# Performance work log

Hardware: AMD Instinct MI355X
Metric: run time of the kernel (lower is better)

Reference implementation:

```python
import jax, jax.numpy as jnp
import numpy as np

BN_EPS = 1e-5
LEAKY_SLOPE = 0.2


def setup_inputs() -> dict:
    key = jax.random.key(0)
    B, T, J, H = 32, 128, 24, 256
    ks = jax.random.split(key, 16)

    def w(k, shape, scale=0.05):
        return jax.random.normal(k, shape, dtype=jnp.float32) * scale

    return {
        "xt_seq": jax.random.normal(ks[0], (B, T, J * 3), dtype=jnp.float32),
        "tau_seq": jax.random.uniform(ks[1], (B, T, 1), dtype=jnp.float32),
        "z_seq": jax.random.normal(ks[2], (B, T, H), dtype=jnp.float32),
        "h_n": jax.random.normal(ks[3], (1, B, H), dtype=jnp.float32),
        "adj": jax.random.uniform(ks[4], (J, J), dtype=jnp.float32),
        # linear weights stored as [in, out] (transposed vs torch)
        "w_joint": w(ks[5], (3, H)), "b_joint": jnp.zeros((H,), jnp.float32),
        "w_t1": w(ks[6], (1, H)), "b_t1": jnp.zeros((H,), jnp.float32),
        "w_t2": w(ks[7], (H, H)), "b_t2": jnp.zeros((H,), jnp.float32),
        "w_radar": w(ks[8], (H, H)), "b_radar": jnp.zeros((H,), jnp.float32),
        "w_gcn": w(ks[9], (H, H)), "b_gcn": jnp.zeros((H,), jnp.float32),
        "w_conv": w(ks[10], (H, H, 3)), "b_conv": jnp.zeros((H,), jnp.float32),  # [out,in,k]
        "bn_gamma": jnp.ones((H,), jnp.float32), "bn_beta": jnp.zeros((H,), jnp.float32),
        "bn_mean": jnp.zeros((H,), jnp.float32), "bn_var": jnp.ones((H,), jnp.float32),
        "w_out": w(ks[11], (H, 3)), "b_out": jnp.zeros((3,), jnp.float32),
    }


def _forward(xt_seq, tau_seq, z_seq, h_n, adj,
             w_joint, b_joint, w_t1, b_t1, w_t2, b_t2,
             w_radar, b_radar, w_gcn, b_gcn, w_conv, b_conv,
             bn_gamma, bn_beta, bn_mean, bn_var, w_out, b_out):
    B, T, _ = xt_seq.shape
    J = adj.shape[0]
    H = w_radar.shape[0]

    x = xt_seq.reshape(B, T, J, 3)
    h = x @ w_joint + b_joint                                  # [B,T,J,H]

    t_emb = jax.nn.silu(tau_seq @ w_t1 + b_t1) @ w_t2 + b_t2   # [B,T,H]
    h = h + t_emb[:, :, None, :]

    z_proj = z_seq @ w_radar + b_radar                         # [B,T,H]
    h = h + z_proj[:, :, None, :]

    h_radar = h_n[0] @ w_radar + b_radar                       # [B,H]
    h = h + h_radar[:, None, None, :]

    # GCN adjacency aggregation + linear + relu residual
    h_gcn = jnp.einsum('jk,btkh->btjh', adj, h)
    h = h + jax.nn.relu(h_gcn @ w_gcn + b_gcn)

    # temporal conv over T: [B*J, H, T]
    h_t = h.transpose(0, 2, 3, 1).reshape(B * J, H, T)
    h_t = jax.lax.conv_general_dilated(
        h_t, w_conv, window_strides=(1,), padding=[(1, 1)],
        dimension_numbers=('NCH', 'OIH', 'NCH')) + b_conv[None, :, None]
    # BatchNorm1d in eval mode (running stats)
    scale = bn_gamma * jax.lax.rsqrt(bn_var + BN_EPS)
    h_t = (h_t - bn_mean[None, :, None]) * scale[None, :, None] + bn_beta[None, :, None]
    h_t = jnp.where(h_t >= 0, h_t, LEAKY_SLOPE * h_t)

    h = h_t.reshape(B, J, H, T).transpose(0, 3, 1, 2)          # [B,T,J,H]
    v = h @ w_out + b_out                                      # [B,T,J,3]
    return v.reshape(B, T, -1)


def reference(xt_seq, tau_seq, z_seq, h_n, adj,
              w_joint, b_joint, w_t1, b_t1, w_t2, b_t2,
              w_radar, b_radar, w_gcn, b_gcn, w_conv, b_conv,
              bn_gamma, bn_beta, bn_mean, bn_var, w_out, b_out):
    return _forward(xt_seq, tau_seq, z_seq, h_n, adj,
                    w_joint, b_joint, w_t1, b_t1, w_t2, b_t2,
                    w_radar, b_radar, w_gcn, b_gcn, w_conv, b_conv,
                    bn_gamma, bn_beta, bn_mean, bn_var, w_out, b_out)
```

## Files before the change

kernel.cpp:

```cpp
#include <hip/hip_runtime.h>

typedef __attribute__((ext_vector_type(8))) short short8v;
typedef __attribute__((ext_vector_type(4))) float float4v;
typedef unsigned short u16;

constexpr int B_ = 32, T_ = 128, J_ = 24, H_ = 256;
constexpr int BT_ = B_ * T_;
constexpr int M_  = BT_ * J_;
constexpr float BN_EPS_ = 1e-5f, SLOPE_ = 0.2f;

constexpr size_t OB_HGB  = 0;
constexpr size_t OB_HB   = OB_HGB + (size_t)M_ * H_ * 2;
constexpr size_t OB_BASE = OB_HB  + (size_t)M_ * H_ * 2;
constexpr size_t OB_S    = OB_BASE + (size_t)BT_ * H_ * 4;
constexpr size_t OB_WTF  = OB_S + (size_t)BT_ * H_ * 4;
constexpr size_t OB_WGF  = OB_WTF + 768 * 256 * 2;
constexpr size_t OB_HR   = OB_WGF + 256 * 256 * 2;
constexpr size_t OB_BNSC = OB_HR + (size_t)B_ * H_ * 4;
constexpr size_t OB_BNSH = OB_BNSC + 256 * 4;

__device__ __forceinline__ u16 f2b(float f) {
  union { float f; unsigned u; } v; v.f = f;
  return (u16)((v.u + 0x7fffu + ((v.u >> 16) & 1u)) >> 16);
}
__device__ __forceinline__ float b2f(u16 u) {
  union { unsigned u; float f; } v; v.u = ((unsigned)u) << 16; return v.f;
}

__global__ __launch_bounds__(256) void k_misc(
    const float* __restrict__ tau, const float* __restrict__ w_t1,
    const float* __restrict__ b_t1, const float* __restrict__ gamma,
    const float* __restrict__ beta, const float* __restrict__ mean,
    const float* __restrict__ var, float* __restrict__ s,
    float* __restrict__ bnsc, float* __restrict__ bnsh) {
  int bid = blockIdx.x, tid = threadIdx.x;
  float tv = tau[bid];
  float v = tv * w_t1[tid] + b_t1[tid];
  s[bid * H_ + tid] = v / (1.f + expf(-v));
  if (bid == 0) {
    float sc = gamma[tid] * rsqrtf(var[tid] + BN_EPS_);
    bnsc[tid] = sc;
    bnsh[tid] = beta[tid] - mean[tid] * sc;
  }
}

__global__ __launch_bounds__(64) void k_pack(
    const float* __restrict__ w_conv, const float* __restrict__ w_gcn,
    u16* __restrict__ wtf, u16* __restrict__ wgf) {
  int bid = blockIdx.x, l = threadIdx.x;
  int col = (l & 15), kbase = (l >> 4) * 8;
  if (bid < 384) {
    int kb = bid >> 4, nblk = bid & 15;
    int o = nblk * 16 + col;
    u16* dst = wtf + (size_t)bid * 512 + l * 8;
#pragma unroll
    for (int j = 0; j < 8; ++j) {
      int k = kb * 32 + kbase + j;
      int tap = k >> 8, i = k & 255;
      dst[j] = f2b(w_conv[o * 768 + i * 3 + tap]);
    }
  } else {
    int b2 = bid - 384;
    int kb = b2 >> 4, nblk = b2 & 15;
    int o = nblk * 16 + col;
    u16* dst = wgf + (size_t)b2 * 512 + l * 8;
#pragma unroll
    for (int j = 0; j < 8; ++j) {
      int k = kb * 32 + kbase + j;
      dst[j] = f2b(w_gcn[k * 256 + o]);
    }
  }
}

__global__ __launch_bounds__(256) void k_hr(
    const float* __restrict__ hn, const float* __restrict__ w_radar,
    const float* __restrict__ b_radar, float* __restrict__ hr) {
  __shared__ float hs[H_];
  int b = blockIdx.x, c = threadIdx.x;
  hs[c] = hn[b * H_ + c];
  __syncthreads();
  float acc = b_radar[c];
  for (int k = 0; k < H_; ++k) acc += hs[k] * w_radar[k * H_ + c];
  hr[b * H_ + c] = acc;
}

__global__ __launch_bounds__(256) void k_base(
    const float* __restrict__ s, const float* __restrict__ z,
    const float* __restrict__ w_t2, const float* __restrict__ w_radar,
    const float* __restrict__ b_t2, const float* __restrict__ b_radar,
    const float* __restrict__ hr, float* __restrict__ basep) {
  __shared__ float As[16][40];
  __shared__ float Bs[16][128];
  int bm = blockIdx.x & 127, bn = blockIdx.x >> 7;
  int row0 = bm * 32, col0 = bn * 128;
  int tid = threadIdx.x, ty = tid >> 5, tx = tid & 31;
  float acc[4][4] = {};
  for (int ck = 0; ck < 32; ++ck) {
    const float* A = (ck < 16) ? s : z;
    const float* W = (ck < 16) ? w_t2 : w_radar;
    int k0 = (ck & 15) * 16;
    if (tid < 128) {
      int r = tid >> 2, q = tid & 3;
      float4 v = *(const float4*)&A[(row0 + r) * H_ + k0 + q * 4];
      As[q * 4 + 0][r] = v.x; As[q * 4 + 1][r] = v.y;
      As[q * 4 + 2][r] = v.z; As[q * 4 + 3][r] = v.w;
    }
#pragma unroll
    for (int p = 0; p < 2; ++p) {
      int idx = tid + p * 256;
      int br = idx >> 5, c4 = idx & 31;
      *(float4*)&Bs[br][c4 * 4] = *(const float4*)&W[(k0 + br) * H_ + col0 + c4 * 4];
    }
    __syncthreads();
#pragma unroll
    for (int kk = 0; kk < 16; ++kk) {
      float4 av = *(const float4*)&As[kk][ty * 4];
      float4 bv = *(const float4*)&Bs[kk][tx * 4];
      float a[4] = {av.x, av.y, av.z, av.w};
      float b[4] = {bv.x, bv.y, bv.z, bv.w};
#pragma unroll
      for (int i = 0; i < 4; ++i)
#pragma unroll
        for (int j = 0; j < 4; ++j) acc[i][j] += a[i] * b[j];
    }
    __syncthreads();
  }
#pragma unroll
  for (int i = 0; i < 4; ++i) {
    int bt = row0 + ty * 4 + i;
    int b = bt >> 7;
    int c = col0 + tx * 4;
    float4 o;
    o.x = acc[i][0] + b_t2[c + 0] + b_radar[c + 0] + hr[b * H_ + c + 0];
    o.y = acc[i][1] + b_t2[c + 1] + b_radar[c + 1] + hr[b * H_ + c + 1];
    o.z = acc[i][2] + b_t2[c + 2] + b_radar[c + 2] + hr[b * H_ + c + 2];
    o.w = acc[i][3] + b_t2[c + 3] + b_radar[c + 3] + hr[b * H_ + c + 3];
    *(float4*)&basep[bt * H_ + c] = o;
  }
}

__global__ __launch_bounds__(256) void k_hg(
    const float* __restrict__ xt, const float* __restrict__ basep,
    const float* __restrict__ adj, const float* __restrict__ w_joint,
    const float* __restrict__ b_joint, u16* __restrict__ hgb,
    u16* __restrict__ hb) {
  __shared__ float xs[J_ * 3];
  int bt = blockIdx.x, c = threadIdx.x;
  if (c < J_ * 3) xs[c] = xt[bt * (J_ * 3) + c];
  __syncthreads();
  float wj0 = w_joint[c], wj1 = w_joint[H_ + c], wj2 = w_joint[2 * H_ + c];
  float hbase = b_joint[c] + basep[bt * H_ + c];
  float hv[J_];
#pragma unroll
  for (int j = 0; j < J_; ++j) {
    hv[j] = xs[j * 3] * wj0 + xs[j * 3 + 1] * wj1 + xs[j * 3 + 2] * wj2 + hbase;
    hb[(size_t)(bt * J_ + j) * H_ + c] = f2b(hv[j]);
  }
  float acc[J_];
#pragma unroll
  for (int j = 0; j < J_; ++j) acc[j] = 0.f;
  for (int kp = 0; kp < J_; ++kp) {
    float hvk = hv[kp];
#pragma unroll
    for (int j = 0; j < J_; ++j) acc[j] += adj[j * J_ + kp] * hvk;
  }
#pragma unroll
  for (int j = 0; j < J_; ++j) hgb[(size_t)(bt * J_ + j) * H_ + c] = f2b(acc[j]);
}


#define DO_MFMA(A_, B_) do {                                              \
  _Pragma("unroll") for (int mi_ = 0; mi_ < 4; ++mi_)                     \
  _Pragma("unroll") for (int ni_ = 0; ni_ < 4; ++ni_)                     \
    acc[mi_][ni_] = __builtin_amdgcn_mfma_f32_16x16x32_bf16(              \
        A_[mi_], B_[ni_], acc[mi_][ni_], 0, 0, 0);                        \
} while (0)

__global__ __launch_bounds__(256) void k_gcn3(
    const u16* __restrict__ wgf, const float* __restrict__ b_gcn,
    const u16* __restrict__ hb, u16* __restrict__ hgb) {
  __shared__ u16 Asm[64 * 256];
  int tid = threadIdx.x;
  int l = tid & 63, wn = tid >> 6;
  int l15 = l & 15, hi16 = (l >> 4) * 16, l8 = l * 8;
  int bid = blockIdx.x;
  int swz = (bid & 7) * 192 + (bid >> 3);
  int r0 = swz * 64;
  char* ab = (char*)Asm;

#pragma unroll
  for (int p = 0; p < 8; ++p) {
    int c = tid + p * 256;
    int lr = c >> 5, c16 = c & 31;
    short8v v = *(const short8v*)&hgb[(size_t)(r0 + lr) * 256 + c16 * 8];
    int off = (lr * 512 + c16 * 16) ^ ((lr & 7) << 4);
    *(short8v*)(ab + off) = v;
  }
  __syncthreads();

  float4v z4 = {0.f, 0.f, 0.f, 0.f};
  float4v acc[4][4];
#pragma unroll
  for (int mi = 0; mi < 4; ++mi)
#pragma unroll
    for (int ni = 0; ni < 4; ++ni) acc[mi][ni] = z4;

  const u16* wbase = wgf + (size_t)wn * 4 * 512 + l8;

#define LB_G(dst, kb) do {                                                \
  const u16* bp_ = wbase + (size_t)(kb) * 16 * 512;                       \
  _Pragma("unroll") for (int ni_ = 0; ni_ < 4; ++ni_)                     \
    dst[ni_] = *(const short8v*)(bp_ + ni_ * 512);                        \
} while (0)
#define LA_G(dst, kb) do {                                                \
  _Pragma("unroll") for (int mi_ = 0; mi_ < 4; ++mi_) {                   \
    int lr_ = mi_ * 16 + l15;                                             \
    int off_ = (lr_ * 512 + (kb) * 64 + hi16) ^ ((lr_ & 7) << 4);         \
    dst[mi_] = *(const short8v*)(ab + off_);                              \
  }                                                                       \
} while (0)

  short8v a0[4], a1[4], b0[4], b1[4];
  LB_G(b0, 0); LB_G(b1, 1); LA_G(a0, 0); LA_G(a1, 1);
#pragma unroll
  for (int kb2 = 0; kb2 < 8; kb2 += 2) {
    DO_MFMA(a0, b0);
    if (kb2 + 2 < 8) { LB_G(b0, kb2 + 2); LA_G(a0, kb2 + 2); }
    DO_MFMA(a1, b1);
    if (kb2 + 3 < 8) { LB_G(b1, kb2 + 3); LA_G(a1, kb2 + 3); }
  }
#undef LB_G
#undef LA_G

  int g = l >> 4;
#pragma unroll
  for (int ni = 0; ni < 4; ++ni) {
    int col = wn * 64 + ni * 16 + l15;
    float bg = b_gcn[col];
#pragma unroll
    for (int mi = 0; mi < 4; ++mi)
#pragma unroll
      for (int r = 0; r < 4; ++r) {
        int row = r0 + mi * 16 + g * 4 + r;
        float hres = b2f(hb[(size_t)row * 256 + col]);
        float gv = acc[mi][ni][r] + bg;
        hgb[(size_t)row * 256 + col] = f2b(hres + (gv > 0.f ? gv : 0.f));
      }
  }
}

__global__ __launch_bounds__(256) void k_conv3(
    const u16* __restrict__ wtf, const float* __restrict__ b_conv,
    const float* __restrict__ bnsc, const float* __restrict__ bnsh,
    const float* __restrict__ w_out, const float* __restrict__ b_out,
    const u16* __restrict__ h2b, float* __restrict__ vout) {
  __shared__ u16 Asm[112 * 256];
  __shared__ float pvbuf[4][64][3];
  int tid = threadIdx.x;
  int l = tid & 63, wn = tid >> 6;
  int l15 = l & 15, hi16 = (l >> 4) * 16, l8 = l * 8;
  int bid = blockIdx.x;
  int swz = (bid & 7) * 192 + (bid >> 3);
  int r0 = swz * 64;
  char* ab = (char*)Asm;

#pragma unroll
  for (int p = 0; p < 14; ++p) {
    int c = tid + p * 256;
    int lr = c >> 5, c16 = c & 31;
    int grow = r0 - 24 + lr;
    grow = grow < 0 ? 0 : (grow >= M_ ? M_ - 1 : grow);
    short8v v = *(const short8v*)&h2b[(size_t)grow * 256 + c16 * 8];
    int off = (lr * 512 + c16 * 16) ^ ((lr & 7) << 4);
    *(short8v*)(ab + off) = v;
  }
  __syncthreads();

  int t0[4];
#pragma unroll
  for (int mi = 0; mi < 4; ++mi) {
    int row = r0 + mi * 16 + l15;
    t0[mi] = (row / 24) & 127;
  }
  short8v z8 = {0, 0, 0, 0, 0, 0, 0, 0};

  float4v z4 = {0.f, 0.f, 0.f, 0.f};
  float4v acc[4][4];
#pragma unroll
  for (int mi = 0; mi < 4; ++mi)
#pragma unroll
    for (int ni = 0; ni < 4; ++ni) acc[mi][ni] = z4;

  const u16* wbase = wtf + (size_t)wn * 4 * 512 + l8;

#define LB_C(dst, kb) do {                                                \
  const u16* bp_ = wbase + (size_t)(kb) * 16 * 512;                       \
  _Pragma("unroll") for (int ni_ = 0; ni_ < 4; ++ni_)                     \
    dst[ni_] = *(const short8v*)(bp_ + ni_ * 512);                        \
} while (0)
#define LA_C(dst, kb) do {                                                \
  int tap_ = (kb) >> 3;                                                   \
  _Pragma("unroll") for (int mi_ = 0; mi_ < 4; ++mi_) {                   \
    int lr_ = tap_ * 24 + mi_ * 16 + l15;                                 \
    int off_ = (lr_ * 512 + ((kb) & 7) * 64 + hi16) ^ ((lr_ & 7) << 4);   \
    short8v v_ = *(const short8v*)(ab + off_);                            \
    if (tap_ != 1) {                                                      \
      bool ok_ = (unsigned)(t0[mi_] + tap_ - 1) < 128u;                   \
      v_ = ok_ ? v_ : z8;                                                 \
    }                                                                     \
    dst[mi_] = v_;                                                        \
  }                                                                       \
} while (0)

  short8v a0[4], a1[4], b0[4], b1[4];
  LB_C(b0, 0); LB_C(b1, 1); LA_C(a0, 0); LA_C(a1, 1);
#pragma unroll
  for (int kb2 = 0; kb2 < 24; kb2 += 2) {
    DO_MFMA(a0, b0);
    if (kb2 + 2 < 24) { LB_C(b0, kb2 + 2); LA_C(a0, kb2 + 2); }
    DO_MFMA(a1, b1);
    if (kb2 + 3 < 24) { LB_C(b1, kb2 + 3); LA_C(a1, kb2 + 3); }
  }
#undef LB_C
#undef LA_C

  float pv[4][4][3] = {};
#pragma unroll
  for (int ni = 0; ni < 4; ++ni) {
    int col = wn * 64 + ni * 16 + l15;
    float bc = b_conv[col], scv = bnsc[col], shv = bnsh[col];
    float w0v = w_out[col * 3], w1v = w_out[col * 3 + 1], w2v = w_out[col * 3 + 2];
#pragma unroll
    for (int mi = 0; mi < 4; ++mi)
#pragma unroll
      for (int r = 0; r < 4; ++r) {
        float hv = acc[mi][ni][r] + bc;
        hv = hv * scv + shv;
        hv = (hv >= 0.f) ? hv : SLOPE_ * hv;
        pv[mi][r][0] += hv * w0v;
        pv[mi][r][1] += hv * w1v;
        pv[mi][r][2] += hv * w2v;
      }
  }
#pragma unroll
  for (int mi = 0; mi < 4; ++mi)
#pragma unroll
    for (int r = 0; r < 4; ++r)
#pragma unroll
      for (int c = 0; c < 3; ++c) {
        float v = pv[mi][r][c];
        v += __shfl_xor(v, 1);
        v += __shfl_xor(v, 2);
        v += __shfl_xor(v, 4);
        v += __shfl_xor(v, 8);
        pv[mi][r][c] = v;
      }
  int g = l >> 4;
  if (l15 == 0) {
#pragma unroll
    for (int mi = 0; mi < 4; ++mi)
#pragma unroll
      for (int r = 0; r < 4; ++r) {
        int rl = mi * 16 + g * 4 + r;
        pvbuf[wn][rl][0] = pv[mi][r][0];
        pvbuf[wn][rl][1] = pv[mi][r][1];
        pvbuf[wn][rl][2] = pv[mi][r][2];
      }
  }
  __syncthreads();
  if (tid < 192) {
    int row = tid / 3, c = tid - row * 3;
    float sum = pvbuf[0][row][c] + pvbuf[1][row][c] + pvbuf[2][row][c] +
                pvbuf[3][row][c] + b_out[c];
    vout[(size_t)(r0 + row) * 3 + c] = sum;
  }
}

extern "C" void kernel_launch(void* const* d_in, const int* in_sizes, int n_in,
                              void* d_out, int out_size, void* d_ws, size_t ws_size,
                              hipStream_t stream) {
  (void)in_sizes; (void)n_in; (void)out_size; (void)ws_size;
  const float* xt      = (const float*)d_in[0];
  const float* tau     = (const float*)d_in[1];
  const float* z       = (const float*)d_in[2];
  const float* hn      = (const float*)d_in[3];
  const float* adj     = (const float*)d_in[4];
  const float* w_joint = (const float*)d_in[5];
  const float* b_joint = (const float*)d_in[6];
  const float* w_t1    = (const float*)d_in[7];
  const float* b_t1    = (const float*)d_in[8];
  const float* w_t2    = (const float*)d_in[9];
  const float* b_t2    = (const float*)d_in[10];
  const float* w_radar = (const float*)d_in[11];
  const float* b_radar = (const float*)d_in[12];
  const float* w_gcn   = (const float*)d_in[13];
  const float* b_gcn   = (const float*)d_in[14];
  const float* w_conv  = (const float*)d_in[15];
  const float* b_conv  = (const float*)d_in[16];
  const float* gamma   = (const float*)d_in[17];
  const float* beta    = (const float*)d_in[18];
  const float* mean    = (const float*)d_in[19];
  const float* var     = (const float*)d_in[20];
  const float* w_out   = (const float*)d_in[21];
  const float* b_out   = (const float*)d_in[22];

  char* wsb = (char*)d_ws;
  u16*   hgb   = (u16*)(wsb + OB_HGB);
  u16*   hbres = (u16*)(wsb + OB_HB);
  float* base  = (float*)(wsb + OB_BASE);
  float* s     = (float*)(wsb + OB_S);
  u16*   wtf   = (u16*)(wsb + OB_WTF);
  u16*   wgf   = (u16*)(wsb + OB_WGF);
  float* hr    = (float*)(wsb + OB_HR);
  float* bnsc  = (float*)(wsb + OB_BNSC);
  float* bnsh  = (float*)(wsb + OB_BNSH);
  float* vout  = (float*)d_out;

  hipLaunchKernelGGL(k_misc, dim3(BT_), dim3(256), 0, stream,
                     tau, w_t1, b_t1, gamma, beta, mean, var, s, bnsc, bnsh);
  hipLaunchKernelGGL(k_pack, dim3(512), dim3(64), 0, stream, w_conv, w_gcn, wtf, wgf);
  hipLaunchKernelGGL(k_hr, dim3(B_), dim3(256), 0, stream, hn, w_radar, b_radar, hr);
  hipLaunchKernelGGL(k_base, dim3(256), dim3(256), 0, stream,
                     s, z, w_t2, w_radar, b_t2, b_radar, hr, base);
  hipLaunchKernelGGL(k_hg, dim3(BT_), dim3(256), 0, stream,
                     xt, base, adj, w_joint, b_joint, hgb, hbres);
  hipLaunchKernelGGL(k_gcn3, dim3(M_ / 64), dim3(256), 0, stream,
                     wgf, b_gcn, hbres, hgb);
  hipLaunchKernelGGL(k_conv3, dim3(M_ / 64), dim3(256), 0, stream,
                     wtf, b_conv, bnsc, bnsh, w_out, b_out, hgb, vout);
}
```

Measured before the change: 274.6 us.

## Fuse front-end kernels into one and pack weights through LDS

Merges the time-embedding, radar projection, hidden-state projection, joint embedding and adjacency aggregation into a single kernel that handles 8 timesteps per block. The fused kernel folds h_n into z before the shared w_radar product, which removes the separate hr kernel. The intermediate base and s buffers are no longer round-tripped through global memory, and bf16 outputs are staged in LDS so they can be written with vectorized coalesced stores. Weight packing and the BN constant setup now run in one small kernel that stages weights in LDS. This cuts the launch count from seven to four, at the cost of a scalar-FMA fp32 GEMM with only 512 blocks and heavy LDS use per block.

```diff
diff --git a/kernel.cpp b/kernel.cpp
--- a/kernel.cpp
+++ b/kernel.cpp
@@ -11,12 +11,9 @@
 
 constexpr size_t OB_HGB  = 0;
 constexpr size_t OB_HB   = OB_HGB + (size_t)M_ * H_ * 2;
-constexpr size_t OB_BASE = OB_HB  + (size_t)M_ * H_ * 2;
-constexpr size_t OB_S    = OB_BASE + (size_t)BT_ * H_ * 4;
-constexpr size_t OB_WTF  = OB_S + (size_t)BT_ * H_ * 4;
+constexpr size_t OB_WTF  = OB_HB  + (size_t)M_ * H_ * 2;
 constexpr size_t OB_WGF  = OB_WTF + 768 * 256 * 2;
-constexpr size_t OB_HR   = OB_WGF + 256 * 256 * 2;
-constexpr size_t OB_BNSC = OB_HR + (size_t)B_ * H_ * 4;
+constexpr size_t OB_BNSC = OB_WGF + 256 * 256 * 2;
 constexpr size_t OB_BNSH = OB_BNSC + 256 * 4;
 
 __device__ __forceinline__ u16 f2b(float f) {
@@ -27,147 +24,174 @@
   union { unsigned u; float f; } v; v.u = ((unsigned)u) << 16; return v.f;
 }
 
-__global__ __launch_bounds__(256) void k_misc(
-    const float* __restrict__ tau, const float* __restrict__ w_t1,
-    const float* __restrict__ b_t1, const float* __restrict__ gamma,
-    const float* __restrict__ beta, const float* __restrict__ mean,
-    const float* __restrict__ var, float* __restrict__ s,
+__global__ __launch_bounds__(256) void k_pack2(
+    const float* __restrict__ w_conv, const float* __restrict__ w_gcn,
+    const float* __restrict__ gamma, const float* __restrict__ beta,
+    const float* __restrict__ mean, const float* __restrict__ var,
+    u16* __restrict__ wtf, u16* __restrict__ wgf,
     float* __restrict__ bnsc, float* __restrict__ bnsh) {
+  __shared__ float wlds[12288];
   int bid = blockIdx.x, tid = threadIdx.x;
-  float tv = tau[bid];
-  float v = tv * w_t1[tid] + b_t1[tid];
-  s[bid * H_ + tid] = v / (1.f + expf(-v));
-  if (bid == 0) {
+  if (bid < 16) {
+    int nblk = bid, o0 = nblk * 16;
+#pragma unroll
+    for (int p = 0; p < 12; ++p) {
+      int lin = tid + p * 256;
+      int row = lin / 192, c4 = lin % 192;
+      *(float4*)&wlds[row * 768 + c4 * 4] =
+          *(const float4*)&w_conv[(size_t)(o0 + row) * 768 + c4 * 4];
+    }
+    __syncthreads();
+#pragma unroll
+    for (int p = 0; p < 6; ++p) {
+      int unit = tid + p * 256;
+      int kb = unit >> 6, l = unit & 63;
+      int col = l & 15, kb8 = (l >> 4) * 8;
+      u16 tmp[8];
+#pragma unroll
+      for (int j = 0; j < 8; ++j) {
+        int k = kb * 32 + kb8 + j;
+        int tap = k >> 8, i = k & 255;
+        tmp[j] = f2b(wlds[col * 768 + i * 3 + tap]);
+      }
+      *(short8v*)&wtf[((size_t)kb * 16 + nblk) * 512 + l * 8] = *(short8v*)tmp;
+    }
+  } else if (bid < 24) {
+    int kb = bid - 16;
+#pragma unroll
+    for (int p = 0; p < 8; ++p) {
+      int lin = tid + p * 256;
+      int row = lin >> 6, c4 = lin & 63;
+      *(float4*)&wlds[row * 256 + c4 * 4] =
+          *(const float4*)&w_gcn[((size_t)kb * 32 + row) * 256 + c4 * 4];
+    }
+    __syncthreads();
+#pragma unroll
+    for (int p = 0; p < 4; ++p) {
+      int unit = tid + p * 256;
+      int nblk = unit >> 6, l = unit & 63;
+      int col = l & 15, kb8 = (l >> 4) * 8;
+      u16 tmp[8];
+#pragma unroll
+      for (int j = 0; j < 8; ++j)
+        tmp[j] = f2b(wlds[(kb8 + j) * 256 + nblk * 16 + col]);
+      *(short8v*)&wgf[((size_t)kb * 16 + nblk) * 512 + l * 8] = *(short8v*)tmp;
+    }
+  } else {
     float sc = gamma[tid] * rsqrtf(var[tid] + BN_EPS_);
     bnsc[tid] = sc;
     bnsh[tid] = beta[tid] - mean[tid] * sc;
   }
 }
 
-__global__ __launch_bounds__(64) void k_pack(
-    const float* __restrict__ w_conv, const float* __restrict__ w_gcn,
-    u16* __restrict__ wtf, u16* __restrict__ wgf) {
-  int bid = blockIdx.x, l = threadIdx.x;
-  int col = (l & 15), kbase = (l >> 4) * 8;
-  if (bid < 384) {
-    int kb = bid >> 4, nblk = bid & 15;
-    int o = nblk * 16 + col;
-    u16* dst = wtf + (size_t)bid * 512 + l * 8;
-#pragma unroll
-    for (int j = 0; j < 8; ++j) {
-      int k = kb * 32 + kbase + j;
-      int tap = k >> 8, i = k & 255;
-      dst[j] = f2b(w_conv[o * 768 + i * 3 + tap]);
-    }
-  } else {
-    int b2 = bid - 384;
-    int kb = b2 >> 4, nblk = b2 & 15;
-    int o = nblk * 16 + col;
-    u16* dst = wgf + (size_t)b2 * 512 + l * 8;
-#pragma unroll
-    for (int j = 0; j < 8; ++j) {
-      int k = kb * 32 + kbase + j;
-      dst[j] = f2b(w_gcn[k * 256 + o]);
-    }
-  }
-}
-
-__global__ __launch_bounds__(256) void k_hr(
-    const float* __restrict__ hn, const float* __restrict__ w_radar,
-    const float* __restrict__ b_radar, float* __restrict__ hr) {
-  __shared__ float hs[H_];
-  int b = blockIdx.x, c = threadIdx.x;
-  hs[c] = hn[b * H_ + c];
+__global__ __launch_bounds__(256) void k_front(
+    const float* __restrict__ xt, const float* __restrict__ tau,
+    const float* __restrict__ z, const float* __restrict__ hn,
+    const float* __restrict__ adj, const float* __restrict__ w_joint,
+    const float* __restrict__ b_joint, const float* __restrict__ w_t1,
+    const float* __restrict__ b_t1, const float* __restrict__ w_t2,
+    const float* __restrict__ b_t2, const float* __restrict__ w_radar,
+    const float* __restrict__ b_radar,
+    u16* __restrict__ hgb, u16* __restrict__ hb) {
+  __shared__ float Af[8][512];
+  __shared__ float basel[8][256];
+  __shared__ float xall[8][72];
+  __shared__ __align__(16) u16 hstage[2][24][256];
+  int tid = threadIdx.x;
+  int bt0 = blockIdx.x * 8;
+  int b = bt0 >> 7;
+
+  {
+    float w1 = w_t1[tid], bb1 = b_t1[tid];
+#pragma unroll
+    for (int r = 0; r < 8; ++r) {
+      float v = tau[bt0 + r] * w1 + bb1;
+      Af[r][tid] = v / (1.f + expf(-v));
+    }
+    float4 hnv = *(const float4*)&hn[(size_t)b * 256 + (tid & 63) * 4];
+#pragma unroll
+    for (int p = 0; p < 2; ++p) {
+      int lin = tid + p * 256;
+      int r = lin >> 6, c4 = lin & 63;
+      float4 zv = *(const float4*)&z[(size_t)(bt0 + r) * 256 + c4 * 4];
+      *(float4*)&Af[r][256 + c4 * 4] =
+          make_float4(zv.x + hnv.x, zv.y + hnv.y, zv.z + hnv.z, zv.w + hnv.w);
+    }
+    if (tid < 144) {
+      *(float4*)&((float*)xall)[tid * 4] =
+          *(const float4*)&xt[(size_t)bt0 * 72 + tid * 4];
+    }
+  }
   __syncthreads();
-  float acc = b_radar[c];
-  for (int k = 0; k < H_; ++k) acc += hs[k] * w_radar[k * H_ + c];
-  hr[b * H_ + c] = acc;
-}
-
-__global__ __launch_bounds__(256) void k_base(
-    const float* __restrict__ s, const float* __restrict__ z,
-    const float* __restrict__ w_t2, const float* __restrict__ w_radar,
-    const float* __restrict__ b_t2, const float* __restrict__ b_radar,
-    const float* __restrict__ hr, float* __restrict__ basep) {
-  __shared__ float As[16][40];
-  __shared__ float Bs[16][128];
-  int bm = blockIdx.x & 127, bn = blockIdx.x >> 7;
-  int row0 = bm * 32, col0 = bn * 128;
-  int tid = threadIdx.x, ty = tid >> 5, tx = tid & 31;
-  float acc[4][4] = {};
-  for (int ck = 0; ck < 32; ++ck) {
-    const float* A = (ck < 16) ? s : z;
-    const float* W = (ck < 16) ? w_t2 : w_radar;
-    int k0 = (ck & 15) * 16;
-    if (tid < 128) {
-      int r = tid >> 2, q = tid & 3;
-      float4 v = *(const float4*)&A[(row0 + r) * H_ + k0 + q * 4];
-      As[q * 4 + 0][r] = v.x; As[q * 4 + 1][r] = v.y;
-      As[q * 4 + 2][r] = v.z; As[q * 4 + 3][r] = v.w;
-    }
-#pragma unroll
-    for (int p = 0; p < 2; ++p) {
-      int idx = tid + p * 256;
-      int br = idx >> 5, c4 = idx & 31;
-      *(float4*)&Bs[br][c4 * 4] = *(const float4*)&W[(k0 + br) * H_ + col0 + c4 * 4];
-    }
+
+  int ty = tid >> 6, tx = tid & 63;
+  float acc[2][4] = {};
+#pragma unroll 1
+  for (int half = 0; half < 2; ++half) {
+    const float* W = half ? w_radar : w_t2;
+    int kbase = half * 256;
+#pragma unroll 8
+    for (int k = 0; k < 256; ++k) {
+      float4 bv = *(const float4*)&W[(size_t)k * 256 + tx * 4];
+      float a0 = Af[2 * ty + 0][kbase + k];
+      float a1 = Af[2 * ty + 1][kbase + k];
+      acc[0][0] += a0 * bv.x; acc[0][1] += a0 * bv.y;
+      acc[0][2] += a0 * bv.z; acc[0][3] += a0 * bv.w;
+      acc[1][0] += a1 * bv.x; acc[1][1] += a1 * bv.y;
+      acc[1][2] += a1 * bv.z; acc[1][3] += a1 * bv.w;
+    }
+  }
+  {
+    float4 bt2v = *(const float4*)&b_t2[tx * 4];
+    float4 brv  = *(const float4*)&b_radar[tx * 4];
+#pragma unroll
+    for (int i = 0; i < 2; ++i) {
+      *(float4*)&basel[2 * ty + i][tx * 4] =
+          make_float4(acc[i][0] + bt2v.x + brv.x, acc[i][1] + bt2v.y + brv.y,
+                      acc[i][2] + bt2v.z + brv.z, acc[i][3] + bt2v.w + brv.w);
+    }
+  }
+  __syncthreads();
+
+  float wj0 = w_joint[tid], wj1 = w_joint[256 + tid], wj2 = w_joint[512 + tid];
+  float bj = b_joint[tid];
+  for (int r = 0; r < 8; ++r) {
+    float hbase = bj + basel[r][tid];
+    float hv[24];
+#pragma unroll
+    for (int j = 0; j < 24; ++j) {
+      hv[j] = xall[r][3 * j] * wj0 + xall[r][3 * j + 1] * wj1 +
+              xall[r][3 * j + 2] * wj2 + hbase;
+      hstage[0][j][tid] = f2b(hv[j]);
+    }
+    float ag[24] = {};
+#pragma unroll
+    for (int kp = 0; kp < 24; ++kp) {
+      float hvk = hv[kp];
+#pragma unroll
+      for (int j = 0; j < 24; ++j) ag[j] += adj[j * 24 + kp] * hvk;
+    }
+#pragma unroll
+    for (int j = 0; j < 24; ++j) hstage[1][j][tid] = f2b(ag[j]);
     __syncthreads();
-#pragma unroll
-    for (int kk = 0; kk < 16; ++kk) {
-      float4 av = *(const float4*)&As[kk][ty * 4];
-      float4 bv = *(const float4*)&Bs[kk][tx * 4];
-      float a[4] = {av.x, av.y, av.z, av.w};
-      float b[4] = {bv.x, bv.y, bv.z, bv.w};
-#pragma unroll
-      for (int i = 0; i < 4; ++i)
-#pragma unroll
-        for (int j = 0; j < 4; ++j) acc[i][j] += a[i] * b[j];
+    size_t gro = (size_t)(bt0 + r) * 24 * 256;
+#pragma unroll
+    for (int p = 0; p < 3; ++p) {
+      int uu = tid + p * 256;
+      int j = uu >> 5, c8 = uu & 31;
+      *(short8v*)&hb[gro + j * 256 + c8 * 8] =
+          *(const short8v*)&hstage[0][j][c8 * 8];
+    }
+#pragma unroll
+    for (int p = 0; p < 3; ++p) {
+      int uu = tid + p * 256;
+      int j = uu >> 5, c8 = uu & 31;
+      *(short8v*)&hgb[gro + j * 256 + c8 * 8] =
+          *(const short8v*)&hstage[1][j][c8 * 8];
     }
     __syncthreads();
   }
-#pragma unroll
-  for (int i = 0; i < 4; ++i) {
-    int bt = row0 + ty * 4 + i;
-    int b = bt >> 7;
-    int c = col0 + tx * 4;
-    float4 o;
-    o.x = acc[i][0] + b_t2[c + 0] + b_radar[c + 0] + hr[b * H_ + c + 0];
-    o.y = acc[i][1] + b_t2[c + 1] + b_radar[c + 1] + hr[b * H_ + c + 1];
-    o.z = acc[i][2] + b_t2[c + 2] + b_radar[c + 2] + hr[b * H_ + c + 2];
-    o.w = acc[i][3] + b_t2[c + 3] + b_radar[c + 3] + hr[b * H_ + c + 3];
-    *(float4*)&basep[bt * H_ + c] = o;
-  }
-}
-
-__global__ __launch_bounds__(256) void k_hg(
-    const float* __restrict__ xt, const float* __restrict__ basep,
-    const float* __restrict__ adj, const float* __restrict__ w_joint,
-    const float* __restrict__ b_joint, u16* __restrict__ hgb,
-    u16* __restrict__ hb) {
-  __shared__ float xs[J_ * 3];
-  int bt = blockIdx.x, c = threadIdx.x;
-  if (c < J_ * 3) xs[c] = xt[bt * (J_ * 3) + c];
-  __syncthreads();
-  float wj0 = w_joint[c], wj1 = w_joint[H_ + c], wj2 = w_joint[2 * H_ + c];
-  float hbase = b_joint[c] + basep[bt * H_ + c];
-  float hv[J_];
-#pragma unroll
-  for (int j = 0; j < J_; ++j) {
-    hv[j] = xs[j * 3] * wj0 + xs[j * 3 + 1] * wj1 + xs[j * 3 + 2] * wj2 + hbase;
-    hb[(size_t)(bt * J_ + j) * H_ + c] = f2b(hv[j]);
-  }
-  float acc[J_];
-#pragma unroll
-  for (int j = 0; j < J_; ++j) acc[j] = 0.f;
-  for (int kp = 0; kp < J_; ++kp) {
-    float hvk = hv[kp];
-#pragma unroll
-    for (int j = 0; j < J_; ++j) acc[j] += adj[j * J_ + kp] * hvk;
-  }
-#pragma unroll
-  for (int j = 0; j < J_; ++j) hgb[(size_t)(bt * J_ + j) * H_ + c] = f2b(acc[j]);
-}
-
+}
 
 #define DO_MFMA(A_, B_) do {                                              \
   _Pragma("unroll") for (int mi_ = 0; mi_ < 4; ++mi_)                     \
@@ -407,23 +431,17 @@
   char* wsb = (char*)d_ws;
   u16*   hgb   = (u16*)(wsb + OB_HGB);
   u16*   hbres = (u16*)(wsb + OB_HB);
-  float* base  = (float*)(wsb + OB_BASE);
-  float* s     = (float*)(wsb + OB_S);
   u16*   wtf   = (u16*)(wsb + OB_WTF);
   u16*   wgf   = (u16*)(wsb + OB_WGF);
-  float* hr    = (float*)(wsb + OB_HR);
   float* bnsc  = (float*)(wsb + OB_BNSC);
   float* bnsh  = (float*)(wsb + OB_BNSH);
   float* vout  = (float*)d_out;
 
-  hipLaunchKernelGGL(k_misc, dim3(BT_), dim3(256), 0, stream,
-                     tau, w_t1, b_t1, gamma, beta, mean, var, s, bnsc, bnsh);
-  hipLaunchKernelGGL(k_pack, dim3(512), dim3(64), 0, stream, w_conv, w_gcn, wtf, wgf);
-  hipLaunchKernelGGL(k_hr, dim3(B_), dim3(256), 0, stream, hn, w_radar, b_radar, hr);
-  hipLaunchKernelGGL(k_base, dim3(256), dim3(256), 0, stream,
-                     s, z, w_t2, w_radar, b_t2, b_radar, hr, base);
-  hipLaunchKernelGGL(k_hg, dim3(BT_), dim3(256), 0, stream,
-                     xt, base, adj, w_joint, b_joint, hgb, hbres);
+  hipLaunchKernelGGL(k_pack2, dim3(25), dim3(256), 0, stream,
+                     w_conv, w_gcn, gamma, beta, mean, var, wtf, wgf, bnsc, bnsh);
+  hipLaunchKernelGGL(k_front, dim3(512), dim3(256), 0, stream,
+                     xt, tau, z, hn, adj, w_joint, b_joint, w_t1, b_t1,
+                     w_t2, b_t2, w_radar, b_radar, hgb, hbres);
   hipLaunchKernelGGL(k_gcn3, dim3(M_ / 64), dim3(256), 0, stream,
                      wgf, b_gcn, hbres, hgb);
   hipLaunchKernelGGL(k_conv3, dim3(M_ / 64), dim3(256), 0, stream,
```

Result: slower. 476.2 us (+73.4%).
